# Optimization experiments

Measured on AMD Instinct MI355X. Metric: run time of the kernel, lower is better.

The kernel has to match this reference:

```python
import jax, jax.numpy as jnp
import numpy as np
import math

NUM_HEADS = 16
HEAD_SIZE = 64
BLOCK = 64          # SLA block size for pooled block scores / sparse selection
TOPK_RATIO = 0.1    # fraction of KV blocks attended per query block


def setup_inputs() -> dict:
    key = jax.random.key(0)
    kq, kk, kv = jax.random.split(key, 3)
    B, S, HD = 2, 4096, NUM_HEADS * HEAD_SIZE
    return {
        "query": jax.random.normal(kq, (B, S, HD), dtype=jnp.float32),
        "key": jax.random.normal(kk, (B, S, HD), dtype=jnp.float32),
        "value": jax.random.normal(kv, (B, S, HD), dtype=jnp.float32),
    }


def _sla_attention(q, k, v):
    # q, k, v: (B, H, S, D). Block-topk sparse attention (SLA-style):
    # mean-pool q/k per block, score blocks, keep top-k key blocks per
    # query block, gather only those K/V blocks, softmax over them.
    B, H, S, D = q.shape
    Nb = S // BLOCK
    scale = 1.0 / math.sqrt(D)

    qb = q.reshape(B, H, Nb, BLOCK, D)
    kb = k.reshape(B, H, Nb, BLOCK, D)
    vb = v.reshape(B, H, Nb, BLOCK, D)

    q_pool = qb.mean(axis=3)  # (B,H,Nb,D)
    k_pool = kb.mean(axis=3)  # (B,H,Nb,D)
    block_scores = jnp.einsum("bhid,bhjd->bhij", q_pool, k_pool) * scale

    K = max(1, int(math.ceil(TOPK_RATIO * Nb)))
    _, idx = jax.lax.top_k(block_scores, K)  # (B,H,Nb,K) selected key blocks

    # Gather selected key/value blocks: (B,H,Nb,K,BLOCK,D)
    gather_idx = idx[..., None, None]
    k_sel = jnp.take_along_axis(kb[:, :, None], gather_idx, axis=3)
    v_sel = jnp.take_along_axis(vb[:, :, None], gather_idx, axis=3)

    # Per-query-block scores over the K*BLOCK selected keys
    scores = jnp.einsum("bhnqd,bhnkjd->bhnqkj", qb, k_sel) * scale
    scores = scores.reshape(B, H, Nb, BLOCK, K * BLOCK)
    probs = jax.nn.softmax(scores, axis=-1)

    v_flat = v_sel.reshape(B, H, Nb, K * BLOCK, D)
    out = jnp.einsum("bhnqk,bhnkd->bhnqd", probs, v_flat)
    return out.reshape(B, H, S, D)


def reference(query, key, value):
    B, S, HD = query.shape
    H, D = NUM_HEADS, HEAD_SIZE
    # b s (h d) -> b h s d
    q = query.reshape(B, S, H, D).transpose(0, 2, 1, 3)
    k = key.reshape(B, S, H, D).transpose(0, 2, 1, 3)
    v = value.reshape(B, S, H, D).transpose(0, 2, 1, 3)
    out = _sla_attention(q, k, v)  # (B,H,S,D)
    # b h s d -> b s (h d)
    return out.transpose(0, 2, 1, 3).reshape(B, S, HD)
```

## Files before the change

### kernel.cpp

```cpp
#include <hip/hip_runtime.h>

constexpr int Bn = 2;
constexpr int Sn = 4096;
constexpr int Hh = 16;
constexpr int Dn = 64;
constexpr int HD = 1024;
constexpr int NB = 64;
constexpr int KS = 7;

typedef _Float16 f16x8 __attribute__((ext_vector_type(8)));
typedef _Float16 f16x4 __attribute__((ext_vector_type(4)));
typedef float    f32x4 __attribute__((ext_vector_type(4)));

static __device__ __forceinline__ f16x4 cvt4(float4 v) {
    f16x4 r;
    r[0] = (_Float16)v.x; r[1] = (_Float16)v.y;
    r[2] = (_Float16)v.z; r[3] = (_Float16)v.w;
    return r;
}

__global__ __launch_bounds__(64) void sla_pool(const float* __restrict__ Q,
                                               const float* __restrict__ K,
                                               float* __restrict__ qpool,
                                               float* __restrict__ kpool) {
    int bid = blockIdx.x;
    int b   = bid / (Hh * NB);
    int rem = bid % (Hh * NB);
    int h   = rem / NB;
    int nb  = rem % NB;
    int d   = threadIdx.x;

    const float* qp = Q + ((size_t)b * Sn + (size_t)nb * 64) * HD + h * Dn + d;
    const float* kp = K + ((size_t)b * Sn + (size_t)nb * 64) * HD + h * Dn + d;
    double sq = 0.0, sk = 0.0;
    #pragma unroll 16
    for (int r = 0; r < 64; ++r) {
        sq += (double)qp[(size_t)r * HD];
        sk += (double)kp[(size_t)r * HD];
    }
    qpool[(size_t)bid * 64 + d] = (float)(sq * (1.0 / 64.0));
    kpool[(size_t)bid * 64 + d] = (float)(sk * (1.0 / 64.0));
}

__global__ __launch_bounds__(64) void sla_topk(const float* __restrict__ qpool,
                                               const float* __restrict__ kpool,
                                               int* __restrict__ topk) {
    int bid = blockIdx.x;
    int bh  = bid / NB;
    int j   = threadIdx.x;

    const float* qp = qpool + (size_t)bid * 64;
    const float* kp = kpool + ((size_t)bh * NB + j) * 64;
    double s = 0.0;
    #pragma unroll 8
    for (int d = 0; d < 64; ++d) s += (double)qp[d] * (double)kp[d];

    double v  = s;
    int   idx = j;
    #pragma unroll
    for (int it = 0; it < KS; ++it) {
        double bv = v; int bi = idx;
        #pragma unroll
        for (int off = 1; off < 64; off <<= 1) {
            double ov = __shfl_xor(bv, off);
            int    oi = __shfl_xor(bi, off);
            if (ov > bv || (ov == bv && oi < bi)) { bv = ov; bi = oi; }
        }
        if (j == 0) topk[(size_t)bid * KS + it] = bi;
        if (idx == bi) v = -1e300;
    }
}

__global__ __launch_bounds__(256) void sla_attn(const float* __restrict__ Q,
                                                const float* __restrict__ K,
                                                const float* __restrict__ V,
                                                const int* __restrict__ topk,
                                                float* __restrict__ O) {
    __shared__ _Float16 Ks[64][72];
    __shared__ _Float16 Vt[64][72];
    __shared__ _Float16 Pl[4][16][72];

    int raw = blockIdx.x;
    int bid = (raw & 7) * 256 + (raw >> 3);

    int b   = bid / (Hh * NB);
    int rem = bid % (Hh * NB);
    int h   = rem / NB;
    int nb  = rem % NB;

    int tid  = threadIdx.x;
    int w    = tid >> 6;
    int lane = tid & 63;
    int c    = lane & 15;
    int g    = lane >> 4;

    int skey = tid >> 2;
    int sdg  = (tid & 3) << 4;
    int vcol = skey ^ ((tid & 3) << 4);

    int jidx[KS];
    {
        const int* tkp = topk + (size_t)bid * KS;
        #pragma unroll
        for (int i = 0; i < KS; ++i) jidx[i] = tkp[i];
    }

    f16x8 qf[2];
    {
        const float* qrow = Q + ((size_t)b * Sn + (size_t)nb * 64 + w * 16 + c) * HD + h * Dn;
        #pragma unroll
        for (int s2 = 0; s2 < 2; ++s2) {
            float4 a0 = *(const float4*)(qrow + s2 * 32 + g * 8);
            float4 a1 = *(const float4*)(qrow + s2 * 32 + g * 8 + 4);
            f16x8 q;
            q[0] = (_Float16)(a0.x * 0.125f); q[1] = (_Float16)(a0.y * 0.125f);
            q[2] = (_Float16)(a0.z * 0.125f); q[3] = (_Float16)(a0.w * 0.125f);
            q[4] = (_Float16)(a1.x * 0.125f); q[5] = (_Float16)(a1.y * 0.125f);
            q[6] = (_Float16)(a1.z * 0.125f); q[7] = (_Float16)(a1.w * 0.125f);
            qf[s2] = q;
        }
    }

    float m[4], l[4];
    f32x4 oacc[4];
    #pragma unroll
    for (int r = 0; r < 4; ++r) { m[r] = -1e30f; l[r] = 0.f; }
    #pragma unroll
    for (int t = 0; t < 4; ++t) oacc[t] = f32x4{0.f, 0.f, 0.f, 0.f};

    const float* kbase = K + (size_t)b * Sn * HD + h * Dn;
    const float* vbase = V + (size_t)b * Sn * HD + h * Dn;

    float4 kx[4], vx[4];
    {
        const float* kp = kbase + ((size_t)jidx[0] * 64 + skey) * HD + sdg;
        const float* vp = vbase + ((size_t)jidx[0] * 64 + skey) * HD + sdg;
        #pragma unroll
        for (int i = 0; i < 4; ++i) kx[i] = *(const float4*)(kp + i * 4);
        #pragma unroll
        for (int i = 0; i < 4; ++i) vx[i] = *(const float4*)(vp + i * 4);
    }

    for (int kb = 0; kb < KS; ++kb) {
        __syncthreads();
        #pragma unroll
        for (int i = 0; i < 4; ++i)
            *(f16x4*)&Ks[skey][sdg + i * 4] = cvt4(kx[i]);
        #pragma unroll
        for (int i = 0; i < 4; ++i) {
            float4 v = vx[i];
            int db = sdg + i * 4;
            Vt[db + 0][vcol] = (_Float16)v.x;
            Vt[db + 1][vcol] = (_Float16)v.y;
            Vt[db + 2][vcol] = (_Float16)v.z;
            Vt[db + 3][vcol] = (_Float16)v.w;
        }
        if (kb + 1 < KS) {
            const float* kp = kbase + ((size_t)jidx[kb + 1] * 64 + skey) * HD + sdg;
            const float* vp = vbase + ((size_t)jidx[kb + 1] * 64 + skey) * HD + sdg;
            #pragma unroll
            for (int i = 0; i < 4; ++i) kx[i] = *(const float4*)(kp + i * 4);
            #pragma unroll
            for (int i = 0; i < 4; ++i) vx[i] = *(const float4*)(vp + i * 4);
        }
        __syncthreads();

        f32x4 sacc[4];
        #pragma unroll
        for (int t = 0; t < 4; ++t) sacc[t] = f32x4{0.f, 0.f, 0.f, 0.f};
        #pragma unroll
        for (int t = 0; t < 4; ++t) {
            #pragma unroll
            for (int s2 = 0; s2 < 2; ++s2) {
                f16x8 bf = *(const f16x8*)&Ks[t * 16 + c][s2 * 32 + g * 8];
                sacc[t] = __builtin_amdgcn_mfma_f32_16x16x32_f16(qf[s2], bf, sacc[t], 0, 0, 0);
            }
        }

        float pm[4];
        #pragma unroll
        for (int r = 0; r < 4; ++r)
            pm[r] = fmaxf(fmaxf(sacc[0][r], sacc[1][r]), fmaxf(sacc[2][r], sacc[3][r]));
        #pragma unroll
        for (int off = 1; off < 16; off <<= 1) {
            #pragma unroll
            for (int r = 0; r < 4; ++r)
                pm[r] = fmaxf(pm[r], __shfl_xor(pm[r], off));
        }
        float al[4], rs[4], pv[4][4];
        #pragma unroll
        for (int r = 0; r < 4; ++r) {
            float mn = fmaxf(m[r], pm[r]);
            al[r] = __expf(m[r] - mn);
            m[r]  = mn;
            rs[r] = 0.f;
        }
        #pragma unroll
        for (int t = 0; t < 4; ++t) {
            #pragma unroll
            for (int r = 0; r < 4; ++r) {
                float e = __expf(sacc[t][r] - m[r]);
                pv[t][r] = e;
                rs[r] += e;
            }
        }
        #pragma unroll
        for (int off = 1; off < 16; off <<= 1) {
            #pragma unroll
            for (int r = 0; r < 4; ++r)
                rs[r] += __shfl_xor(rs[r], off);
        }
        #pragma unroll
        for (int r = 0; r < 4; ++r) l[r] = l[r] * al[r] + rs[r];
        #pragma unroll
        for (int t = 0; t < 4; ++t) {
            #pragma unroll
            for (int r = 0; r < 4; ++r) oacc[t][r] *= al[r];
        }

        #pragma unroll
        for (int t = 0; t < 4; ++t) {
            #pragma unroll
            for (int r = 0; r < 4; ++r)
                Pl[w][g * 4 + r][t * 16 + c] = (_Float16)pv[t][r];
        }

        f16x8 af0 = *(const f16x8*)&Pl[w][c][g * 8];
        f16x8 af1 = *(const f16x8*)&Pl[w][c][32 + g * 8];
        #pragma unroll
        for (int t = 0; t < 4; ++t) {
            int cv0 = (g * 8)      ^ ((t & 3) << 4);
            int cv1 = (32 + g * 8) ^ ((t & 3) << 4);
            f16x8 b0 = *(const f16x8*)&Vt[t * 16 + c][cv0];
            f16x8 b1 = *(const f16x8*)&Vt[t * 16 + c][cv1];
            oacc[t] = __builtin_amdgcn_mfma_f32_16x16x32_f16(af0, b0, oacc[t], 0, 0, 0);
            oacc[t] = __builtin_amdgcn_mfma_f32_16x16x32_f16(af1, b1, oacc[t], 0, 0, 0);
        }
    }

    float* orow = O + ((size_t)b * Sn + (size_t)nb * 64 + w * 16) * HD + h * Dn;
    #pragma unroll
    for (int r = 0; r < 4; ++r) {
        float inv = 1.0f / l[r];
        #pragma unroll
        for (int t = 0; t < 4; ++t)
            orow[(size_t)(g * 4 + r) * HD + t * 16 + c] = oacc[t][r] * inv;
    }
}

extern "C" void kernel_launch(void* const* d_in, const int* in_sizes, int n_in,
                              void* d_out, int out_size, void* d_ws, size_t ws_size,
                              hipStream_t stream) {
    const float* Q = (const float*)d_in[0];
    const float* K = (const float*)d_in[1];
    const float* V = (const float*)d_in[2];
    float* O = (float*)d_out;

    float* qpool = (float*)d_ws;
    float* kpool = qpool + (size_t)Bn * Hh * NB * Dn;
    int*   topk  = (int*)(kpool + (size_t)Bn * Hh * NB * Dn);

    dim3 grid(Bn * Hh * NB);
    sla_pool<<<grid, 64, 0, stream>>>(Q, K, qpool, kpool);
    sla_topk<<<grid, 64, 0, stream>>>(qpool, kpool, topk);
    sla_attn<<<grid, 256, 0, stream>>>(Q, K, V, topk, O);
}
```

Before: 88.32 us.

## Transpose MFMA operand roles so each lane owns one query row

Swaps the A/B operands of both MFMAs so the accumulator holds S^T and O^T, which puts each query row's statistics in a single lane. The softmax max and sum reductions drop from 4-step shuffles over 4 rows to 2 cross-group shuffles on one value, and the output becomes a float4 store per lane. K is stored in shared memory with an XOR chunk swizzle written as 8-wide vectors, and P is written as f16x4 into a smaller padded buffer. This cuts shuffle and scalar LDS traffic but depends on the new swizzle and index mapping being correct.

```diff
diff --git a/kernel.cpp b/kernel.cpp
--- a/kernel.cpp
+++ b/kernel.cpp
@@ -16,6 +16,14 @@
     f16x4 r;
     r[0] = (_Float16)v.x; r[1] = (_Float16)v.y;
     r[2] = (_Float16)v.z; r[3] = (_Float16)v.w;
+    return r;
+}
+static __device__ __forceinline__ f16x8 cvt8(float4 a, float4 b) {
+    f16x8 r;
+    r[0] = (_Float16)a.x; r[1] = (_Float16)a.y;
+    r[2] = (_Float16)a.z; r[3] = (_Float16)a.w;
+    r[4] = (_Float16)b.x; r[5] = (_Float16)b.y;
+    r[6] = (_Float16)b.z; r[7] = (_Float16)b.w;
     return r;
 }
 
@@ -76,9 +84,9 @@
                                                 const float* __restrict__ V,
                                                 const int* __restrict__ topk,
                                                 float* __restrict__ O) {
-    __shared__ _Float16 Ks[64][72];
+    __shared__ _Float16 Ks[64][64];
     __shared__ _Float16 Vt[64][72];
-    __shared__ _Float16 Pl[4][16][72];
+    __shared__ _Float16 Pq[4][16][68];
 
     int raw = blockIdx.x;
     int bid = (raw & 7) * 256 + (raw >> 3);
@@ -95,8 +103,13 @@
     int g    = lane >> 4;
 
     int skey = tid >> 2;
-    int sdg  = (tid & 3) << 4;
-    int vcol = skey ^ ((tid & 3) << 4);
+    int sd3  = tid & 3;
+    int sdg  = sd3 << 4;
+    int vcol = skey ^ (sd3 << 4);
+    int kch0 = ((sd3 << 1) + 0) ^ (skey & 7);
+    int kch1 = ((sd3 << 1) + 1) ^ (skey & 7);
+    int rch0 = (g + 0) ^ (c & 7);
+    int rch1 = (g + 4) ^ (c & 7);
 
     int jidx[KS];
     {
@@ -121,10 +134,8 @@
         }
     }
 
-    float m[4], l[4];
+    float m = -1e30f, l = 0.f;
     f32x4 oacc[4];
-    #pragma unroll
-    for (int r = 0; r < 4; ++r) { m[r] = -1e30f; l[r] = 0.f; }
     #pragma unroll
     for (int t = 0; t < 4; ++t) oacc[t] = f32x4{0.f, 0.f, 0.f, 0.f};
 
@@ -143,9 +154,8 @@
 
     for (int kb = 0; kb < KS; ++kb) {
         __syncthreads();
-        #pragma unroll
-        for (int i = 0; i < 4; ++i)
-            *(f16x4*)&Ks[skey][sdg + i * 4] = cvt4(kx[i]);
+        *(f16x8*)&Ks[skey][kch0 * 8] = cvt8(kx[0], kx[1]);
+        *(f16x8*)&Ks[skey][kch1 * 8] = cvt8(kx[2], kx[3]);
         #pragma unroll
         for (int i = 0; i < 4; ++i) {
             float4 v = vx[i];
@@ -170,81 +180,76 @@
         for (int t = 0; t < 4; ++t) sacc[t] = f32x4{0.f, 0.f, 0.f, 0.f};
         #pragma unroll
         for (int t = 0; t < 4; ++t) {
-            #pragma unroll
-            for (int s2 = 0; s2 < 2; ++s2) {
-                f16x8 bf = *(const f16x8*)&Ks[t * 16 + c][s2 * 32 + g * 8];
-                sacc[t] = __builtin_amdgcn_mfma_f32_16x16x32_f16(qf[s2], bf, sacc[t], 0, 0, 0);
-            }
-        }
-
-        float pm[4];
-        #pragma unroll
-        for (int r = 0; r < 4; ++r)
-            pm[r] = fmaxf(fmaxf(sacc[0][r], sacc[1][r]), fmaxf(sacc[2][r], sacc[3][r]));
-        #pragma unroll
-        for (int off = 1; off < 16; off <<= 1) {
-            #pragma unroll
-            for (int r = 0; r < 4; ++r)
-                pm[r] = fmaxf(pm[r], __shfl_xor(pm[r], off));
-        }
-        float al[4], rs[4], pv[4][4];
-        #pragma unroll
-        for (int r = 0; r < 4; ++r) {
-            float mn = fmaxf(m[r], pm[r]);
-            al[r] = __expf(m[r] - mn);
-            m[r]  = mn;
-            rs[r] = 0.f;
-        }
+            f16x8 a0 = *(const f16x8*)&Ks[t * 16 + c][rch0 * 8];
+            f16x8 a1 = *(const f16x8*)&Ks[t * 16 + c][rch1 * 8];
+            sacc[t] = __builtin_amdgcn_mfma_f32_16x16x32_f16(a0, qf[0], sacc[t], 0, 0, 0);
+            sacc[t] = __builtin_amdgcn_mfma_f32_16x16x32_f16(a1, qf[1], sacc[t], 0, 0, 0);
+        }
+
+        float pm;
+        {
+            float m0 = fmaxf(fmaxf(sacc[0][0], sacc[0][1]), fmaxf(sacc[0][2], sacc[0][3]));
+            float m1 = fmaxf(fmaxf(sacc[1][0], sacc[1][1]), fmaxf(sacc[1][2], sacc[1][3]));
+            float m2 = fmaxf(fmaxf(sacc[2][0], sacc[2][1]), fmaxf(sacc[2][2], sacc[2][3]));
+            float m3 = fmaxf(fmaxf(sacc[3][0], sacc[3][1]), fmaxf(sacc[3][2], sacc[3][3]));
+            pm = fmaxf(fmaxf(m0, m1), fmaxf(m2, m3));
+        }
+        pm = fmaxf(pm, __shfl_xor(pm, 16));
+        pm = fmaxf(pm, __shfl_xor(pm, 32));
+
+        float mn = fmaxf(m, pm);
+        float al = __expf(m - mn);
+        m = mn;
+
+        float e[4][4];
+        float rs = 0.f;
         #pragma unroll
         for (int t = 0; t < 4; ++t) {
             #pragma unroll
             for (int r = 0; r < 4; ++r) {
-                float e = __expf(sacc[t][r] - m[r]);
-                pv[t][r] = e;
-                rs[r] += e;
+                float x = __expf(sacc[t][r] - m);
+                e[t][r] = x;
+                rs += x;
             }
         }
-        #pragma unroll
-        for (int off = 1; off < 16; off <<= 1) {
-            #pragma unroll
-            for (int r = 0; r < 4; ++r)
-                rs[r] += __shfl_xor(rs[r], off);
-        }
-        #pragma unroll
-        for (int r = 0; r < 4; ++r) l[r] = l[r] * al[r] + rs[r];
-        #pragma unroll
-        for (int t = 0; t < 4; ++t) {
-            #pragma unroll
-            for (int r = 0; r < 4; ++r) oacc[t][r] *= al[r];
-        }
-
-        #pragma unroll
-        for (int t = 0; t < 4; ++t) {
-            #pragma unroll
-            for (int r = 0; r < 4; ++r)
-                Pl[w][g * 4 + r][t * 16 + c] = (_Float16)pv[t][r];
-        }
-
-        f16x8 af0 = *(const f16x8*)&Pl[w][c][g * 8];
-        f16x8 af1 = *(const f16x8*)&Pl[w][c][32 + g * 8];
+        rs += __shfl_xor(rs, 16);
+        rs += __shfl_xor(rs, 32);
+        l = l * al + rs;
+        #pragma unroll
+        for (int t = 0; t < 4; ++t) {
+            oacc[t][0] *= al; oacc[t][1] *= al;
+            oacc[t][2] *= al; oacc[t][3] *= al;
+        }
+
+        #pragma unroll
+        for (int t = 0; t < 4; ++t) {
+            f16x4 p4;
+            p4[0] = (_Float16)e[t][0]; p4[1] = (_Float16)e[t][1];
+            p4[2] = (_Float16)e[t][2]; p4[3] = (_Float16)e[t][3];
+            *(f16x4*)&Pq[w][c][t * 16 + g * 4] = p4;
+        }
+
         #pragma unroll
         for (int t = 0; t < 4; ++t) {
             int cv0 = (g * 8)      ^ ((t & 3) << 4);
             int cv1 = (32 + g * 8) ^ ((t & 3) << 4);
-            f16x8 b0 = *(const f16x8*)&Vt[t * 16 + c][cv0];
-            f16x8 b1 = *(const f16x8*)&Vt[t * 16 + c][cv1];
-            oacc[t] = __builtin_amdgcn_mfma_f32_16x16x32_f16(af0, b0, oacc[t], 0, 0, 0);
-            oacc[t] = __builtin_amdgcn_mfma_f32_16x16x32_f16(af1, b1, oacc[t], 0, 0, 0);
-        }
-    }
-
-    float* orow = O + ((size_t)b * Sn + (size_t)nb * 64 + w * 16) * HD + h * Dn;
+            f16x8 va0 = *(const f16x8*)&Vt[t * 16 + c][cv0];
+            f16x8 va1 = *(const f16x8*)&Vt[t * 16 + c][cv1];
+            f16x8 pa0 = *(const f16x8*)&Pq[w][c][g * 8];
+            f16x8 pa1 = *(const f16x8*)&Pq[w][c][32 + g * 8];
+            oacc[t] = __builtin_amdgcn_mfma_f32_16x16x32_f16(va0, pa0, oacc[t], 0, 0, 0);
+            oacc[t] = __builtin_amdgcn_mfma_f32_16x16x32_f16(va1, pa1, oacc[t], 0, 0, 0);
+        }
+    }
+
+    float inv = 1.0f / l;
+    float* orow = O + ((size_t)b * Sn + (size_t)nb * 64 + w * 16 + c) * HD + h * Dn;
     #pragma unroll
-    for (int r = 0; r < 4; ++r) {
-        float inv = 1.0f / l[r];
-        #pragma unroll
-        for (int t = 0; t < 4; ++t)
-            orow[(size_t)(g * 4 + r) * HD + t * 16 + c] = oacc[t][r] * inv;
+    for (int t = 0; t < 4; ++t) {
+        float4 o4;
+        o4.x = oacc[t][0] * inv; o4.y = oacc[t][1] * inv;
+        o4.z = oacc[t][2] * inv; o4.w = oacc[t][3] * inv;
+        *(float4*)(orow + t * 16 + g * 4) = o4;
     }
 }
 
```

Measured after the change: 73.59 us. -16.7%, faster.
